# Performance work log

Hardware: AMD Instinct MI355X
Metric: run time of the kernel (lower is better)

The kernel has to match this reference:

```python
import jax, jax.numpy as jnp
import numpy as np

_SQRT4PI = float(np.sqrt(4.0 * np.pi))

def spherical_harmonics_l2(vec):
    # e3nn real spherical harmonics, lmax=2, normalize=True, normalization='integral'
    # component-normalized values divided by sqrt(4*pi); e3nn (x,y,z) ordering with y as zenith
    r = jnp.linalg.norm(vec, axis=-1, keepdims=True)
    u = vec / jnp.maximum(r, 1e-12)
    x, y, z = u[..., 0], u[..., 1], u[..., 2]
    c1 = np.float32(np.sqrt(3.0)); c2 = np.float32(np.sqrt(15.0)); c3 = np.float32(np.sqrt(5.0))
    sh = jnp.stack([
        jnp.ones_like(x),                      # l=0
        c1 * x, c1 * y, c1 * z,                # l=1
        c2 * x * z,                            # l=2
        c2 * x * y,
        c3 * (y * y - 0.5 * (x * x + z * z)),
        c2 * y * z,
        (c2 * 0.5) * (z * z - x * x),
    ], axis=-1)
    return sh * np.float32(1.0 / _SQRT4PI)

def setup_inputs() -> dict:
    key = jax.random.key(0)
    ks = jax.random.split(key, 8)
    N, M, C, F, SH = 50000, 12, 128, 64, 9
    return dict(
        atom_fea=jax.random.normal(ks[0], (N, C), jnp.float32),
        nbr_fea=jax.random.normal(ks[1], (N, M, F), jnp.float32),
        nbr_idx=jax.random.randint(ks[2], (N, M), 0, N),
        pos=jax.random.normal(ks[3], (N, 3), jnp.float32),
        w1=jax.random.normal(ks[4], (F, F), jnp.float32) * np.float32(1.0 / np.sqrt(F)),
        b1=jnp.zeros((F,), jnp.float32),
        w2=jax.random.normal(ks[5], (F, SH), jnp.float32) * np.float32(1.0 / np.sqrt(F)),
        b2=jnp.zeros((SH,), jnp.float32),
        tp_w=jax.random.normal(ks[6], (C, C), jnp.float32),  # FCTP weight, path (Cx0e)x(1x0e)->(Cx0e)
        bn_gamma=jnp.ones((C,), jnp.float32),
        bn_beta=jnp.zeros((C,), jnp.float32),
    )

def reference(atom_fea, nbr_fea, nbr_idx, pos, w1, b1, w2, b2, tp_w, bn_gamma, bn_beta):
    N, M, F = nbr_fea.shape
    C = atom_fea.shape[1]
    src = nbr_idx.reshape(-1)                                  # (E,)
    h_j = atom_fea[src]                                        # (E, C) gather
    # radial MLP: Linear -> Softplus -> Linear
    R = jax.nn.softplus(nbr_fea.reshape(N * M, F) @ w1 + b1) @ w2 + b2   # (E, 9)
    rel = pos[src] - jnp.repeat(pos, M, axis=0)                # (E, 3), dst = arange(N) repeated M times
    Y = spherical_harmonics_l2(rel)                            # (E, 9)
    W = R * Y                                                  # (E, 9)
    # FullyConnectedTensorProduct(Cx0e, 0e+1o+2e, Cx0e): only 0e x 0e -> 0e path survives,
    # fan-in normalization alpha = 1/sqrt(C)
    msg = (h_j @ tp_w) * W[:, :1] * np.float32(1.0 / np.sqrt(C))  # (E, C)
    # scatter-mean over dst: dst rows are contiguous blocks of size M per node
    agg = msg.reshape(N, M, C).mean(axis=1)                    # (N, C)
    x = atom_fea + agg
    # BatchNorm1d (training-mode batch statistics, eps=1e-5)
    mean = x.mean(axis=0)
    var = x.var(axis=0)
    xn = (x - mean) * jax.lax.rsqrt(var + 1e-5)
    return jax.nn.softplus(bn_gamma * xn + bn_beta)
```

## Files before the change

kernel.cpp:

```cpp
#include <hip/hip_runtime.h>
#include <hip/hip_bf16.h>
#include <cstddef>

#define N_NODES 50000
#define M_NBR   12
#define C_CH    128
#define F_DIM   64
#define E_EDGES (N_NODES * M_NBR)
#define TILES_PER_WAVE 5
#define NBLK_A  1875
#define NBLK_Y  782
#define NBLK_G  782

constexpr float SCALE_CE =
    (float)(1.0 / (3.5449077018110318 * 11.313708498984761 * 12.0));

typedef __bf16 bf16x8 __attribute__((ext_vector_type(8)));
typedef float  f32x4  __attribute__((ext_vector_type(4)));

__device__ __forceinline__ float softplus_f(float x) {
    const float t = __builtin_amdgcn_exp2f(-fabsf(x) * 1.44269504f);
    return fmaxf(x, 0.0f) + 0.69314718f * __builtin_amdgcn_logf(1.0f + t);
}

__device__ __forceinline__ float bfhi_to_f(unsigned int p) {
    return __uint_as_float(p & 0xffff0000u);
}
__device__ __forceinline__ float bflo_to_f(unsigned int p) {
    return __uint_as_float(p << 16);
}

__global__ __launch_bounds__(512) void kW(
    const float* __restrict__ w1,
    const float* __restrict__ tp_w,
    __bf16* __restrict__ fragW1,
    __bf16* __restrict__ fragTP)
{
    const int t = threadIdx.x;
    if (blockIdx.x == 0) {
        const int lane = t & 63;
        const int f = t >> 6;
        const int n = f >> 1, ks = f & 1;
        const int col16 = lane & 15, kgrp = lane >> 4;
        bf16x8 v;
        #pragma unroll
        for (int j = 0; j < 8; ++j)
            v[j] = (__bf16)w1[(ks * 32 + kgrp * 8 + j) * F_DIM + 16 * n + col16];
        *(bf16x8*)&fragW1[(size_t)t * 8] = v;
    } else {
        const int fid = (blockIdx.x - 1) * 512 + t;
        const int lane = fid & 63;
        const int f = fid >> 6;
        const int n = f >> 2, ks = f & 3;
        const int col16 = lane & 15, kgrp = lane >> 4;
        bf16x8 v;
        #pragma unroll
        for (int j = 0; j < 8; ++j)
            v[j] = (__bf16)tp_w[(ks * 32 + kgrp * 8 + j) * C_CH + 16 * n + col16];
        *(bf16x8*)&fragTP[(size_t)fid * 8] = v;
    }
}

__global__ __launch_bounds__(256) void kFront(
    const float* __restrict__ nbr_fea,
    const __bf16* __restrict__ fragW1,
    const float* __restrict__ b1,
    const float* __restrict__ w2,
    const float* __restrict__ b2,
    const float* __restrict__ atom_fea,
    const __bf16* __restrict__ fragTP,
    float* __restrict__ ce,
    __bf16* __restrict__ y)
{
    __shared__ __bf16 yl[64 * 136];
    const int tid   = threadIdx.x;
    const int lane  = tid & 63;
    const int wid   = tid >> 6;
    const int col16 = lane & 15;
    const int kgrp  = lane >> 4;

    if (blockIdx.x < NBLK_A) {
        bf16x8 bfrag[4][2];
        #pragma unroll
        for (int f = 0; f < 8; ++f)
            bfrag[f >> 1][f & 1] = *(const bf16x8*)&fragW1[((size_t)f * 64 + lane) * 8];

        float b1v[4], w2v[4];
        #pragma unroll
        for (int n = 0; n < 4; ++n) {
            b1v[n] = b1[16 * n + col16];
            w2v[n] = w2[(16 * n + col16) * 9];
        }
        const float b2_0 = b2[0];

        const int tile0 = (blockIdx.x * 4 + wid) * TILES_PER_WAVE;
        const float* abase = nbr_fea + ((long)tile0 * 16 + col16) * F_DIM + kgrp * 8;

        float4 c0 = *(const float4*)(abase);
        float4 c1 = *(const float4*)(abase + 4);
        float4 c2 = *(const float4*)(abase + 32);
        float4 c3 = *(const float4*)(abase + 36);

        #pragma unroll
        for (int t = 0; t < TILES_PER_WAVE; ++t) {
            float4 n0, n1, n2, n3;
            if (t + 1 < TILES_PER_WAVE) {
                const float* an = abase + (size_t)(t + 1) * 16 * F_DIM;
                n0 = *(const float4*)(an);
                n1 = *(const float4*)(an + 4);
                n2 = *(const float4*)(an + 32);
                n3 = *(const float4*)(an + 36);
            }

            bf16x8 afrag[2];
            afrag[0][0] = (__bf16)c0.x; afrag[0][1] = (__bf16)c0.y;
            afrag[0][2] = (__bf16)c0.z; afrag[0][3] = (__bf16)c0.w;
            afrag[0][4] = (__bf16)c1.x; afrag[0][5] = (__bf16)c1.y;
            afrag[0][6] = (__bf16)c1.z; afrag[0][7] = (__bf16)c1.w;
            afrag[1][0] = (__bf16)c2.x; afrag[1][1] = (__bf16)c2.y;
            afrag[1][2] = (__bf16)c2.z; afrag[1][3] = (__bf16)c2.w;
            afrag[1][4] = (__bf16)c3.x; afrag[1][5] = (__bf16)c3.y;
            afrag[1][6] = (__bf16)c3.z; afrag[1][7] = (__bf16)c3.w;

            f32x4 acc[4];
            #pragma unroll
            for (int n = 0; n < 4; ++n) acc[n] = (f32x4){0.f, 0.f, 0.f, 0.f};
            #pragma unroll
            for (int ks = 0; ks < 2; ++ks)
                #pragma unroll
                for (int n = 0; n < 4; ++n)
                    acc[n] = __builtin_amdgcn_mfma_f32_16x16x32_bf16(
                        afrag[ks], bfrag[n][ks], acc[n], 0, 0, 0);

            float partial[4] = {0.f, 0.f, 0.f, 0.f};
            #pragma unroll
            for (int n = 0; n < 4; ++n)
                #pragma unroll
                for (int r = 0; r < 4; ++r) {
                    const float h = acc[n][r] + b1v[n];
                    partial[r] = fmaf(softplus_f(h), w2v[n], partial[r]);
                }
            #pragma unroll
            for (int r = 0; r < 4; ++r) {
                #pragma unroll
                for (int off = 1; off <= 8; off <<= 1)
                    partial[r] += __shfl_xor(partial[r], off);
            }
            const long e0 = (long)(tile0 + t) * 16;
            if (col16 == 0) {
                #pragma unroll
                for (int r = 0; r < 4; ++r)
                    ce[e0 + kgrp * 4 + r] = (partial[r] + b2_0) * SCALE_CE;
            }

            c0 = n0; c1 = n1; c2 = n2; c3 = n3;
        }
    } else {
        const int blk  = blockIdx.x - NBLK_A;
        const int row  = blk * 64 + wid * 16 + col16;
        const int rowc = row < N_NODES ? row : N_NODES - 1;
        const float* ap = atom_fea + (size_t)rowc * C_CH + kgrp * 8;

        bf16x8 afrag[4];
        #pragma unroll
        for (int ks = 0; ks < 4; ++ks) {
            float4 f0 = *(const float4*)(ap + ks * 32);
            float4 f1 = *(const float4*)(ap + ks * 32 + 4);
            afrag[ks][0] = (__bf16)f0.x; afrag[ks][1] = (__bf16)f0.y;
            afrag[ks][2] = (__bf16)f0.z; afrag[ks][3] = (__bf16)f0.w;
            afrag[ks][4] = (__bf16)f1.x; afrag[ks][5] = (__bf16)f1.y;
            afrag[ks][6] = (__bf16)f1.z; afrag[ks][7] = (__bf16)f1.w;
        }

        #pragma unroll
        for (int n = 0; n < 8; ++n) {
            f32x4 acc = (f32x4){0.f, 0.f, 0.f, 0.f};
            #pragma unroll
            for (int ks = 0; ks < 4; ++ks) {
                bf16x8 bf = *(const bf16x8*)&fragTP[((size_t)(n * 4 + ks) * 64 + lane) * 8];
                acc = __builtin_amdgcn_mfma_f32_16x16x32_bf16(afrag[ks], bf, acc, 0, 0, 0);
            }
            #pragma unroll
            for (int r = 0; r < 4; ++r)
                yl[(wid * 16 + kgrp * 4 + r) * 136 + 16 * n + col16] = (__bf16)acc[r];
        }
        __syncthreads();

        #pragma unroll
        for (int it = 0; it < 4; ++it) {
            const int e  = it * 2048 + tid * 8;
            const int rw = e >> 7, cl = e & 127;
            const int grow = blk * 64 + rw;
            if (grow < N_NODES) {
                bf16x8 v = *(const bf16x8*)&yl[rw * 136 + cl];
                *(bf16x8*)&y[(size_t)grow * C_CH + cl] = v;
            }
        }
    }
}

__global__ __launch_bounds__(256, 6) void kG(
    const float* __restrict__ atom_fea,
    const __bf16* __restrict__ y,
    const int*   __restrict__ nbr_idx,
    const float* __restrict__ ce,
    unsigned int* __restrict__ xb,
    float* __restrict__ psum,
    float* __restrict__ psumsq)
{
    __shared__ float4 red[4][64];
    const int tid  = threadIdx.x;
    const int lane = tid & 63;
    const int wid  = tid >> 6;
    const int blk  = blockIdx.x;
    const int i0   = blk * 64 + wid * 16;

    float2 sum   = make_float2(0.f, 0.f);
    float2 sumsq = make_float2(0.f, 0.f);

    int   pidx = 0;
    float pce  = 0.f;
    if (i0 < N_NODES && lane < M_NBR) {
        pidx = nbr_idx[i0 * M_NBR + lane];
        pce  = ce[i0 * M_NBR + lane];
    }

    for (int t = 0; t < 16; ++t) {
        const int i = i0 + t;
        const int   cidx = pidx;
        const float cce  = pce;
        const int inext = i + 1;
        if (t < 15 && inext < N_NODES && lane < M_NBR) {
            pidx = nbr_idx[inext * M_NBR + lane];
            pce  = ce[inext * M_NBR + lane];
        }
        if (i < N_NODES) {
            float2 acc = make_float2(0.f, 0.f);
            #pragma unroll
            for (int m = 0; m < M_NBR; ++m) {
                const int   src = __shfl(cidx, m);
                const float c   = __shfl(cce, m);
                const unsigned int p =
                    *(const unsigned int*)(y + (size_t)src * C_CH + lane * 2);
                acc.x = fmaf(c, bflo_to_f(p), acc.x);
                acc.y = fmaf(c, bfhi_to_f(p), acc.y);
            }
            const float2 a = *(const float2*)(atom_fea + (size_t)i * C_CH + lane * 2);
            const float2 xv = make_float2(a.x + acc.x, a.y + acc.y);
            union { __bf16 h[2]; unsigned int u; } pk;
            pk.h[0] = (__bf16)xv.x;
            pk.h[1] = (__bf16)xv.y;
            xb[(size_t)i * 64 + lane] = pk.u;
            sum.x += xv.x; sum.y += xv.y;
            sumsq.x += xv.x * xv.x; sumsq.y += xv.y * xv.y;
        }
    }

    red[wid][lane] = make_float4(sum.x, sum.y, sumsq.x, sumsq.y);
    __syncthreads();
    if (tid < 128) {
        const int l = tid >> 1, comp = tid & 1;
        float s = 0.f, q = 0.f;
        #pragma unroll
        for (int w = 0; w < 4; ++w) {
            const float4 v = red[w][l];
            s += comp ? v.y : v.x;
            q += comp ? v.w : v.z;
        }
        psum[blk * 128 + tid]   = s;
        psumsq[blk * 128 + tid] = q;
    }
}

__global__ __launch_bounds__(1024) void kC1(
    const float* __restrict__ psum,
    const float* __restrict__ psumsq,
    float* __restrict__ mean_o,
    float* __restrict__ istd_o,
    int nblocks)
{
    __shared__ float red[2][8][128];
    const int t = threadIdx.x;
    const int c = t & 127;
    const int grp = t >> 7;
    float s = 0.f, ss = 0.f;
    for (int b = grp; b < nblocks; b += 8) {
        s  += psum[b * 128 + c];
        ss += psumsq[b * 128 + c];
    }
    red[0][grp][c] = s;
    red[1][grp][c] = ss;
    __syncthreads();
    if (t < 128) {
        float S = 0.f, SS = 0.f;
        #pragma unroll
        for (int k = 0; k < 8; ++k) { S += red[0][k][t]; SS += red[1][k][t]; }
        const float m   = S / (float)N_NODES;
        const float var = SS / (float)N_NODES - m * m;
        mean_o[t] = m;
        istd_o[t] = rsqrtf(var + 1e-5f);
    }
}

__global__ __launch_bounds__(256) void kC2(
    const unsigned int* __restrict__ xb,
    float* __restrict__ out,
    const float* __restrict__ mean_i,
    const float* __restrict__ istd_i,
    const float* __restrict__ gamma,
    const float* __restrict__ beta)
{
    __shared__ float sm[128], si[128], sg[128], sb[128];
    const int tid = threadIdx.x;
    if (tid < 128) {
        sm[tid] = mean_i[tid];
        si[tid] = istd_i[tid];
        sg[tid] = gamma[tid];
        sb[tid] = beta[tid];
    }
    __syncthreads();
    const size_t tix = (size_t)blockIdx.x * 256 + tid;
    const uint2 v = *(const uint2*)&xb[tix * 2];
    const int c0 = (int)(tix & 31) * 4;
    float r[4] = {bflo_to_f(v.x), bfhi_to_f(v.x), bflo_to_f(v.y), bfhi_to_f(v.y)};
    float4 o;
    #pragma unroll
    for (int t = 0; t < 4; ++t) {
        const int cc = c0 + t;
        const float xn = (r[t] - sm[cc]) * si[cc];
        r[t] = softplus_f(fmaf(sg[cc], xn, sb[cc]));
    }
    o.x = r[0]; o.y = r[1]; o.z = r[2]; o.w = r[3];
    *(float4*)&out[tix * 4] = o;
}

extern "C" void kernel_launch(void* const* d_in, const int* in_sizes, int n_in,
                              void* d_out, int out_size, void* d_ws, size_t ws_size,
                              hipStream_t stream)
{
    const float* atom_fea = (const float*)d_in[0];
    const float* nbr_fea  = (const float*)d_in[1];
    const int*   nbr_idx  = (const int*)d_in[2];
    const float* w1       = (const float*)d_in[4];
    const float* b1       = (const float*)d_in[5];
    const float* w2       = (const float*)d_in[6];
    const float* b2       = (const float*)d_in[7];
    const float* tp_w     = (const float*)d_in[8];
    const float* bn_gamma = (const float*)d_in[9];
    const float* bn_beta  = (const float*)d_in[10];

    float* out = (float*)d_out;
    float* ws  = (float*)d_ws;

    float* ce      = ws;
    float* psum    = ce + E_EDGES;
    float* psumsq  = psum + (size_t)NBLK_G * 128;
    float* mean_b  = psumsq + (size_t)NBLK_G * 128;
    float* istd_b  = mean_b + 128;
    __bf16* fragW1 = (__bf16*)(istd_b + 128);
    __bf16* fragTP = fragW1 + 4096;
    __bf16* ybuf   = fragTP + 16384;
    unsigned int* xbuf = (unsigned int*)(ybuf + 6400000);

    kW<<<5, 512, 0, stream>>>(w1, tp_w, fragW1, fragTP);
    kFront<<<NBLK_A + NBLK_Y, 256, 0, stream>>>(
        nbr_fea, fragW1, b1, w2, b2, atom_fea, fragTP, ce, ybuf);
    kG<<<NBLK_G, 256, 0, stream>>>(atom_fea, ybuf, nbr_idx, ce,
                                   xbuf, psum, psumsq);
    kC1<<<1, 1024, 0, stream>>>(psum, psumsq, mean_b, istd_b, NBLK_G);
    const int nC2 = (N_NODES * C_CH / 4) / 256;
    kC2<<<nC2, 256, 0, stream>>>(xbuf, out, mean_b, istd_b, bn_gamma, bn_beta);
}
```

Baseline: 112.6 us.

## Stage nbr_fea tiles through LDS with coalesced loads in radial MLP

The radial-MLP part of the front kernel now loads 32-edge super-tiles of nbr_fea with fully coalesced float4 loads into a per-wave padded LDS buffer, then reads the MFMA A-fragments from LDS. Before, each lane read strided rows straight from global memory. Work per wave drops from 5 tiles to 4 (two super-tiles), so the grid grows from 1875 to 2344 blocks. The shared buffer is reused as raw bytes for the other branch. The aim is better global-load coalescing, at the cost of LDS traffic and losing the register prefetch of the next tile.

```diff
diff --git a/kernel.cpp b/kernel.cpp
--- a/kernel.cpp
+++ b/kernel.cpp
@@ -7,8 +7,8 @@
 #define C_CH    128
 #define F_DIM   64
 #define E_EDGES (N_NODES * M_NBR)
-#define TILES_PER_WAVE 5
-#define NBLK_A  1875
+#define NSUP    18750
+#define NBLK_A  2344
 #define NBLK_Y  782
 #define NBLK_G  782
 
@@ -72,7 +72,7 @@
     float* __restrict__ ce,
     __bf16* __restrict__ y)
 {
-    __shared__ __bf16 yl[64 * 136];
+    __shared__ __align__(16) unsigned char smem[4 * 32 * 272];
     const int tid   = threadIdx.x;
     const int lane  = tid & 63;
     const int wid   = tid >> 6;
@@ -93,69 +93,77 @@
         }
         const float b2_0 = b2[0];
 
-        const int tile0 = (blockIdx.x * 4 + wid) * TILES_PER_WAVE;
-        const float* abase = nbr_fea + ((long)tile0 * 16 + col16) * F_DIM + kgrp * 8;
-
-        float4 c0 = *(const float4*)(abase);
-        float4 c1 = *(const float4*)(abase + 4);
-        float4 c2 = *(const float4*)(abase + 32);
-        float4 c3 = *(const float4*)(abase + 36);
-
-        #pragma unroll
-        for (int t = 0; t < TILES_PER_WAVE; ++t) {
-            float4 n0, n1, n2, n3;
-            if (t + 1 < TILES_PER_WAVE) {
-                const float* an = abase + (size_t)(t + 1) * 16 * F_DIM;
-                n0 = *(const float4*)(an);
-                n1 = *(const float4*)(an + 4);
-                n2 = *(const float4*)(an + 32);
-                n3 = *(const float4*)(an + 36);
-            }
-
-            bf16x8 afrag[2];
-            afrag[0][0] = (__bf16)c0.x; afrag[0][1] = (__bf16)c0.y;
-            afrag[0][2] = (__bf16)c0.z; afrag[0][3] = (__bf16)c0.w;
-            afrag[0][4] = (__bf16)c1.x; afrag[0][5] = (__bf16)c1.y;
-            afrag[0][6] = (__bf16)c1.z; afrag[0][7] = (__bf16)c1.w;
-            afrag[1][0] = (__bf16)c2.x; afrag[1][1] = (__bf16)c2.y;
-            afrag[1][2] = (__bf16)c2.z; afrag[1][3] = (__bf16)c2.w;
-            afrag[1][4] = (__bf16)c3.x; afrag[1][5] = (__bf16)c3.y;
-            afrag[1][6] = (__bf16)c3.z; afrag[1][7] = (__bf16)c3.w;
-
-            f32x4 acc[4];
-            #pragma unroll
-            for (int n = 0; n < 4; ++n) acc[n] = (f32x4){0.f, 0.f, 0.f, 0.f};
-            #pragma unroll
-            for (int ks = 0; ks < 2; ++ks)
+        float* S = (float*)(smem + (size_t)wid * 32 * 272);
+        const int sup_base = (blockIdx.x * 4 + wid) * 2;
+
+        #pragma unroll
+        for (int st = 0; st < 2; ++st) {
+            const int sup = sup_base + st;
+            if (sup >= NSUP) break;
+            const long e0 = (long)sup * 32;
+            const float* gsrc = nbr_fea + e0 * F_DIM;
+
+            #pragma unroll
+            for (int i = 0; i < 8; ++i) {
+                const int gi16 = i * 64 + lane;
+                const float4 v = *(const float4*)(gsrc + (size_t)gi16 * 4);
+                const int row = gi16 >> 4;
+                const int u   = gi16 & 15;
+                *(float4*)(S + row * 68 + u * 4) = v;
+            }
+
+            #pragma unroll
+            for (int t = 0; t < 2; ++t) {
+                const float* R = S + (t * 16 + col16) * 68 + kgrp * 8;
+                const float4 a0 = *(const float4*)(R);
+                const float4 a1 = *(const float4*)(R + 4);
+                const float4 a2 = *(const float4*)(R + 32);
+                const float4 a3 = *(const float4*)(R + 36);
+
+                bf16x8 afrag[2];
+                afrag[0][0] = (__bf16)a0.x; afrag[0][1] = (__bf16)a0.y;
+                afrag[0][2] = (__bf16)a0.z; afrag[0][3] = (__bf16)a0.w;
+                afrag[0][4] = (__bf16)a1.x; afrag[0][5] = (__bf16)a1.y;
+                afrag[0][6] = (__bf16)a1.z; afrag[0][7] = (__bf16)a1.w;
+                afrag[1][0] = (__bf16)a2.x; afrag[1][1] = (__bf16)a2.y;
+                afrag[1][2] = (__bf16)a2.z; afrag[1][3] = (__bf16)a2.w;
+                afrag[1][4] = (__bf16)a3.x; afrag[1][5] = (__bf16)a3.y;
+                afrag[1][6] = (__bf16)a3.z; afrag[1][7] = (__bf16)a3.w;
+
+                f32x4 acc[4];
+                #pragma unroll
+                for (int n = 0; n < 4; ++n) acc[n] = (f32x4){0.f, 0.f, 0.f, 0.f};
+                #pragma unroll
+                for (int ks = 0; ks < 2; ++ks)
+                    #pragma unroll
+                    for (int n = 0; n < 4; ++n)
+                        acc[n] = __builtin_amdgcn_mfma_f32_16x16x32_bf16(
+                            afrag[ks], bfrag[n][ks], acc[n], 0, 0, 0);
+
+                float partial[4] = {0.f, 0.f, 0.f, 0.f};
                 #pragma unroll
                 for (int n = 0; n < 4; ++n)
-                    acc[n] = __builtin_amdgcn_mfma_f32_16x16x32_bf16(
-                        afrag[ks], bfrag[n][ks], acc[n], 0, 0, 0);
-
-            float partial[4] = {0.f, 0.f, 0.f, 0.f};
-            #pragma unroll
-            for (int n = 0; n < 4; ++n)
+                    #pragma unroll
+                    for (int r = 0; r < 4; ++r) {
+                        const float h = acc[n][r] + b1v[n];
+                        partial[r] = fmaf(softplus_f(h), w2v[n], partial[r]);
+                    }
                 #pragma unroll
                 for (int r = 0; r < 4; ++r) {
-                    const float h = acc[n][r] + b1v[n];
-                    partial[r] = fmaf(softplus_f(h), w2v[n], partial[r]);
+                    #pragma unroll
+                    for (int off = 1; off <= 8; off <<= 1)
+                        partial[r] += __shfl_xor(partial[r], off);
                 }
-            #pragma unroll
-            for (int r = 0; r < 4; ++r) {
-                #pragma unroll
-                for (int off = 1; off <= 8; off <<= 1)
-                    partial[r] += __shfl_xor(partial[r], off);
-            }
-            const long e0 = (long)(tile0 + t) * 16;
-            if (col16 == 0) {
-                #pragma unroll
-                for (int r = 0; r < 4; ++r)
-                    ce[e0 + kgrp * 4 + r] = (partial[r] + b2_0) * SCALE_CE;
-            }
-
-            c0 = n0; c1 = n1; c2 = n2; c3 = n3;
+                if (col16 == 0) {
+                    const long et = e0 + t * 16;
+                    #pragma unroll
+                    for (int r = 0; r < 4; ++r)
+                        ce[et + kgrp * 4 + r] = (partial[r] + b2_0) * SCALE_CE;
+                }
+            }
         }
     } else {
+        __bf16* yl = (__bf16*)smem;
         const int blk  = blockIdx.x - NBLK_A;
         const int row  = blk * 64 + wid * 16 + col16;
         const int rowc = row < N_NODES ? row : N_NODES - 1;
```

Result: no change. 111.2 us (-1.2%).
